# Optimization experiments

Measured on AMD Instinct MI355X. Metric: run time of the kernel, lower is better.

## Reference

```python
import jax, jax.numpy as jnp
import numpy as np

HIDDEN = 512
HORIZON = 24


def _cell(x, h, c, Wih, Whh, b):
    # PyTorch LSTM cell: gates ordered i, f, g, o; bias = b_ih + b_hh
    z = x @ Wih.T + h @ Whh.T + b  # [B, 4H]
    i, f, g, o = jnp.split(z, 4, axis=-1)
    c = jax.nn.sigmoid(f) * c + jax.nn.sigmoid(i) * jnp.tanh(g)
    h = jax.nn.sigmoid(o) * jnp.tanh(c)
    return h, c


def _run_layer(xs, Wih, Whh, b):
    # xs: [T, B, F] time-major; zero initial state like nn.LSTM
    B = xs.shape[1]
    H = Whh.shape[1]
    h0 = jnp.zeros((B, H), xs.dtype)
    c0 = jnp.zeros((B, H), xs.dtype)

    def step(carry, x_t):
        h, c = carry
        h, c = _cell(x_t, h, c, Wih, Whh, b)
        return (h, c), h

    (hT, cT), hs = jax.lax.scan(step, (h0, c0), xs)
    return hs, hT, cT


def setup_inputs() -> dict:
    key = jax.random.key(0)
    ks = jax.random.split(key, 20)
    s = 1.0 / np.sqrt(HIDDEN)  # torch LSTM/Linear default init scale
    u = lambda k, shape: jax.random.uniform(k, shape, jnp.float32, -s, s)
    B, T, F, H = 512, 256, 8, HIDDEN
    return {
        "x": jax.random.normal(ks[0], (B, T, F), jnp.float32),
        "e_Wih0": u(ks[1], (4 * H, F)),
        "e_Whh0": u(ks[2], (4 * H, H)),
        "e_bih0": u(ks[3], (4 * H,)),
        "e_bhh0": u(ks[4], (4 * H,)),
        "e_Wih1": u(ks[5], (4 * H, H)),
        "e_Whh1": u(ks[6], (4 * H, H)),
        "e_bih1": u(ks[7], (4 * H,)),
        "e_bhh1": u(ks[8], (4 * H,)),
        "d_Wih0": u(ks[9], (4 * H, 1)),
        "d_Whh0": u(ks[10], (4 * H, H)),
        "d_bih0": u(ks[11], (4 * H,)),
        "d_bhh0": u(ks[12], (4 * H,)),
        "d_Wih1": u(ks[13], (4 * H, H)),
        "d_Whh1": u(ks[14], (4 * H, H)),
        "d_bih1": u(ks[15], (4 * H,)),
        "d_bhh1": u(ks[16], (4 * H,)),
        "out_W": u(ks[17], (1, H)),
        "out_b": u(ks[18], (1,)),
    }


def reference(x, e_Wih0, e_Whh0, e_bih0, e_bhh0, e_Wih1, e_Whh1, e_bih1, e_bhh1,
              d_Wih0, d_Whh0, d_bih0, d_bhh0, d_Wih1, d_Whh1, d_bih1, d_bhh1,
              out_W, out_b):
    xs = jnp.swapaxes(x, 0, 1)  # [T, B, F]
    # 2-layer encoder; only final (hidden, cell) per layer are used
    hs0, h0T, c0T = _run_layer(xs, e_Wih0, e_Whh0, e_bih0 + e_bhh0)
    _, h1T, c1T = _run_layer(hs0, e_Wih1, e_Whh1, e_bih1 + e_bhh1)

    dec_in = x[:, -1, 0:1]  # [B, 1] last value of first feature channel

    def dec_step(carry, _):
        h0, c0, h1, c1, inp = carry
        h0, c0 = _cell(inp, h0, c0, d_Wih0, d_Whh0, d_bih0 + d_bhh0)
        h1, c1 = _cell(h0, h1, c1, d_Wih1, d_Whh1, d_bih1 + d_bhh1)
        pred = h1 @ out_W.T + out_b  # [B, 1]
        return (h0, c0, h1, c1, pred), pred

    carry = (h0T, c0T, h1T, c1T, dec_in)
    _, preds = jax.lax.scan(dec_step, carry, None, length=HORIZON)  # [Hz, B, 1]
    return jnp.swapaxes(preds[..., 0], 0, 1)  # [B, Hz]
```

## Files before the change

kernel.cpp:

```cpp
#include <hip/hip_runtime.h>
#include <math.h>

constexpr int H   = 512;
constexpr int B   = 512;
constexpr int T   = 256;
constexpr int F   = 8;
constexpr int HOR = 24;

typedef _Float16 f16;
typedef _Float16 f16x8 __attribute__((ext_vector_type(8)));
typedef float    f32x4 __attribute__((ext_vector_type(4)));

__device__ __forceinline__ float sigm(float x) { return 1.0f / (1.0f + expf(-x)); }

#define LLC_LOAD16S(base, r) \
  asm volatile( \
    "global_load_dwordx4 %0,  %16, off sc0 sc1\n\t" \
    "global_load_dwordx4 %1,  %16, off offset:16 sc0 sc1\n\t" \
    "global_load_dwordx4 %2,  %16, off offset:128 sc0 sc1\n\t" \
    "global_load_dwordx4 %3,  %16, off offset:144 sc0 sc1\n\t" \
    "global_load_dwordx4 %4,  %16, off offset:256 sc0 sc1\n\t" \
    "global_load_dwordx4 %5,  %16, off offset:272 sc0 sc1\n\t" \
    "global_load_dwordx4 %6,  %16, off offset:384 sc0 sc1\n\t" \
    "global_load_dwordx4 %7,  %16, off offset:400 sc0 sc1\n\t" \
    "global_load_dwordx4 %8,  %16, off offset:512 sc0 sc1\n\t" \
    "global_load_dwordx4 %9,  %16, off offset:528 sc0 sc1\n\t" \
    "global_load_dwordx4 %10, %16, off offset:640 sc0 sc1\n\t" \
    "global_load_dwordx4 %11, %16, off offset:656 sc0 sc1\n\t" \
    "global_load_dwordx4 %12, %16, off offset:768 sc0 sc1\n\t" \
    "global_load_dwordx4 %13, %16, off offset:784 sc0 sc1\n\t" \
    "global_load_dwordx4 %14, %16, off offset:896 sc0 sc1\n\t" \
    "global_load_dwordx4 %15, %16, off offset:912 sc0 sc1" \
    : "=v"(r[0]), "=v"(r[1]), "=v"(r[2]), "=v"(r[3]), \
      "=v"(r[4]), "=v"(r[5]), "=v"(r[6]), "=v"(r[7]), \
      "=v"(r[8]), "=v"(r[9]), "=v"(r[10]), "=v"(r[11]), \
      "=v"(r[12]), "=v"(r[13]), "=v"(r[14]), "=v"(r[15]) \
    : "v"(base))

#define VWAIT16(r) \
  asm volatile("s_waitcnt vmcnt(0)" \
    : "+v"(r[0]), "+v"(r[1]), "+v"(r[2]), "+v"(r[3]), \
      "+v"(r[4]), "+v"(r[5]), "+v"(r[6]), "+v"(r[7]), \
      "+v"(r[8]), "+v"(r[9]), "+v"(r[10]), "+v"(r[11]), \
      "+v"(r[12]), "+v"(r[13]), "+v"(r[14]), "+v"(r[15]) :: "memory")

#define LLC_STORE_DWX4(p, v) \
  asm volatile("global_store_dwordx4 %0, %1, off sc0 sc1" :: "v"(p), "v"(v) : "memory")

#define FLAG_STORE(p, v) \
  asm volatile("s_waitcnt vmcnt(0)\n\t" \
               "global_store_dword %0, %1, off sc0 sc1" :: "v"(p), "v"(v) : "memory")

__global__ __launch_bounds__(256)
void wconv_k(const float* __restrict__ s0, f16* __restrict__ d0,
             const float* __restrict__ s1, f16* __restrict__ d1,
             const float* __restrict__ s2, f16* __restrict__ d2,
             const float* __restrict__ s3, f16* __restrict__ d3,
             const float* __restrict__ s4, f16* __restrict__ d4,
             const float* __restrict__ s5, f16* __restrict__ d5)
{
    const float* src; f16* dst;
    switch (blockIdx.y) {
        case 0:  src = s0; dst = d0; break;
        case 1:  src = s1; dst = d1; break;
        case 2:  src = s2; dst = d2; break;
        case 3:  src = s3; dst = d3; break;
        case 4:  src = s4; dst = d4; break;
        default: src = s5; dst = d5; break;
    }
    int idx = (blockIdx.x * 256 + threadIdx.x) * 8;
    int np  = idx >> 9;
    int k   = idx & 511;
    int jh  = np >> 2, g = np & 3;
    const float* sp = src + (size_t)(g * H + jh) * H + k;
    f16 tmp[8];
    #pragma unroll
    for (int j = 0; j < 8; ++j) tmp[j] = (f16)sp[j];
    *(f16x8*)(dst + idx) = *(const f16x8*)tmp;
}

__device__ __forceinline__ void wait_group(const int* f, int target)
{
    if (threadIdx.x < 64) {
        const int* p = f + (threadIdx.x & 31);
        bool ok;
        do {
            int v = target;
            if (threadIdx.x < 32)
                asm volatile("global_load_dword %0, %1, off sc0 sc1\n\t"
                             "s_waitcnt vmcnt(0)"
                             : "=v"(v) : "v"(p) : "memory");
            ok = __all(v >= target);
            if (!ok) __builtin_amdgcn_s_sleep(1);
        } while (!ok);
    }
    __syncthreads();
}

struct WChunk { f16x8 w0, w1; };

__device__ __forceinline__ WChunk loadW(int kt, const f16* __restrict__ W0,
                                        const f16* __restrict__ W1,
                                        int n0, int srow, int sch)
{
    const f16* Wp = (kt < 8) ? W0 : W1;
    const int  ko = ((kt < 8) ? kt : kt - 8) * 64;
    const f16* wp = Wp + (size_t)(n0 + srow) * H + ko + sch * 16;
    WChunk c;
    c.w0 = *(const f16x8*)wp;
    c.w1 = *(const f16x8*)(wp + 8);
    return c;
}

template<int NKT>
__device__ __forceinline__ void cell_body(int bt, int nt, char* smem,
    const f16* __restrict__ A0, const f16* __restrict__ A1,
    const f16* __restrict__ W0, const f16* __restrict__ W1,
    const float* __restrict__ bih, const float* __restrict__ bhh,
    int xmode, const float* __restrict__ xptr, int xstride,
    const float* __restrict__ xw, const float* __restrict__ pred_s,
    float* __restrict__ cst, f16* __restrict__ hout)
{
    constexpr int ABUF = 64 * 72;
    f16*   As = (f16*)smem;
    f16*   Ws = (f16*)smem + 2 * ABUF;
    float* zs = (float*)smem;
    f16*   hstage = (f16*)(smem + 20480);

    const int tid  = threadIdx.x;
    const int lane = tid & 63;
    const int wv   = tid >> 6;
    const int wm   = wv & 1;
    const int wn   = wv >> 1;
    const int r    = lane & 15;
    const int g4   = lane >> 4;
    const int b0   = bt * 64;
    const int n0   = nt * 64;
    const int jh0  = nt * 16;
    const int srow = tid >> 2, sch = tid & 3;

    f32x4 acc[2][2] = {};

    if constexpr (NKT > 0) {
        f16x8 ar[16];
        f16x8 br[16];
        const f16* ap = A0 + (size_t)(b0 + srow) * H + sch * 16;
        LLC_LOAD16S(ap, ar);
        if constexpr (NKT == 16) {
            const f16* bp = A1 + (size_t)(b0 + srow) * H + sch * 16;
            LLC_LOAD16S(bp, br);
        }
        VWAIT16(ar);

        WChunk wcur = loadW(0, W0, W1, n0, srow, sch);
        #pragma unroll
        for (int kt = 0; kt < NKT; ++kt) {
            if (kt == 8) VWAIT16(br);
            f16* Ab = As + (kt & 1) * ABUF;
            f16* Wb = Ws + (kt & 1) * ABUF;
            f16x8 a0v = (kt < 8) ? ar[kt * 2]     : br[(kt - 8) * 2];
            f16x8 a1v = (kt < 8) ? ar[kt * 2 + 1] : br[(kt - 8) * 2 + 1];
            *(f16x8*)(Ab + srow * 72 + sch * 16)     = a0v;
            *(f16x8*)(Ab + srow * 72 + sch * 16 + 8) = a1v;
            *(f16x8*)(Wb + srow * 72 + sch * 16)     = wcur.w0;
            *(f16x8*)(Wb + srow * 72 + sch * 16 + 8) = wcur.w1;
            __syncthreads();

            WChunk wnxt = wcur;
            if (kt + 1 < NKT) wnxt = loadW(kt + 1, W0, W1, n0, srow, sch);

            #pragma unroll
            for (int sub = 0; sub < 2; ++sub) {
                f16x8 bf0 = *(const f16x8*)(Wb + (wn * 32 + r)      * 72 + sub * 32 + g4 * 8);
                f16x8 bf1 = *(const f16x8*)(Wb + (wn * 32 + 16 + r) * 72 + sub * 32 + g4 * 8);
                f16x8 af0 = *(const f16x8*)(Ab + (wm * 32 + r)      * 72 + sub * 32 + g4 * 8);
                f16x8 af1 = *(const f16x8*)(Ab + (wm * 32 + 16 + r) * 72 + sub * 32 + g4 * 8);
                acc[0][0] = __builtin_amdgcn_mfma_f32_16x16x32_f16(af0, bf0, acc[0][0], 0, 0, 0);
                acc[0][1] = __builtin_amdgcn_mfma_f32_16x16x32_f16(af0, bf1, acc[0][1], 0, 0, 0);
                acc[1][0] = __builtin_amdgcn_mfma_f32_16x16x32_f16(af1, bf0, acc[1][0], 0, 0, 0);
                acc[1][1] = __builtin_amdgcn_mfma_f32_16x16x32_f16(af1, bf1, acc[1][1], 0, 0, 0);
            }
            wcur = wnxt;
        }
    }

    __syncthreads();
    #pragma unroll
    for (int fm = 0; fm < 2; ++fm)
        #pragma unroll
        for (int fn = 0; fn < 2; ++fn)
            #pragma unroll
            for (int j = 0; j < 4; ++j)
                zs[(wm * 32 + fm * 16 + g4 * 4 + j) * 68 +
                   (wn * 32 + fn * 16 + r)] = acc[fm][fn][j];
    __syncthreads();

    const int jl = tid & 15;
    const int bq = tid >> 4;
    const int jh = jh0 + jl;

    float bsum[4];
    #pragma unroll
    for (int g = 0; g < 4; ++g) bsum[g] = bih[g * H + jh] + bhh[g * H + jh];

    #pragma unroll
    for (int bb = 0; bb < 4; ++bb) {
        const int bl = bq * 4 + bb;
        const int b  = b0 + bl;
        float4 z = *(const float4*)(zs + bl * 68 + jl * 4);
        float zi = z.x + bsum[0];
        float zf = z.y + bsum[1];
        float zg = z.z + bsum[2];
        float zo = z.w + bsum[3];
        if (xmode == 1) {
            const float* xr = xptr + (size_t)b * xstride;
            #pragma unroll
            for (int k = 0; k < F; ++k) {
                float xv = xr[k];
                zi += xv * xw[(0 * H + jh) * F + k];
                zf += xv * xw[(1 * H + jh) * F + k];
                zg += xv * xw[(2 * H + jh) * F + k];
                zo += xv * xw[(3 * H + jh) * F + k];
            }
        } else if (xmode == 2 || xmode == 3) {
            float xv = (xmode == 2) ? xptr[(size_t)b * xstride] : pred_s[bl];
            zi += xv * xw[0 * H + jh];
            zf += xv * xw[1 * H + jh];
            zg += xv * xw[2 * H + jh];
            zo += xv * xw[3 * H + jh];
        }
        size_t idx = (size_t)b * H + jh;
        float cold = cst[idx];
        float cn = sigm(zf) * cold + sigm(zi) * tanhf(zg);
        cst[idx] = cn;
        hstage[bl * 16 + jl] = (f16)(sigm(zo) * tanhf(cn));
    }
    __syncthreads();
    if (tid < 128) {
        const int row = tid >> 1, half = tid & 1;
        f16x8 hv = *(const f16x8*)(hstage + row * 16 + half * 8);
        f16* hp = hout + (size_t)(b0 + row) * H + jh0 + half * 8;
        LLC_STORE_DWX4(hp, hv);
    }
}

__device__ __forceinline__ void compute_pred(int bt, int nt,
                             const f16* __restrict__ h1src,
                             const float* __restrict__ outW,
                             const float* __restrict__ outb,
                             float* pred_s, float* __restrict__ dout, int oidx)
{
    const int row = threadIdx.x >> 2;
    const int q   = threadIdx.x & 3;
    const int b   = bt * 64 + row;
    const f16x8* hv = (const f16x8*)(h1src + (size_t)b * H + q * 128);
    float s = 0.f;
    #pragma unroll
    for (int k8 = 0; k8 < 16; ++k8) {
        f16x8 h8 = hv[k8];
        const float* wr = outW + q * 128 + k8 * 8;
        #pragma unroll
        for (int j = 0; j < 8; ++j) s += (float)h8[j] * wr[j];
    }
    s += __shfl_down(s, 2);
    s += __shfl_down(s, 1);
    if (q == 0) {
        float p = s + outb[0];
        pred_s[row] = p;
        if (nt == 0) dout[(size_t)b * HOR + oidx] = p;
    }
    __syncthreads();
}

struct PArgs {
    const f16 *wh0, *wih1, *whh1, *dwh0, *dwih1, *dwhh1;
    const float *x;
    const float *ebih0, *ebhh0, *ebih1, *ebhh1;
    const float *dbih0, *dbhh0, *dbih1, *dbhh1;
    const float *eWih0, *dWih0, *outW, *outb;
    f16 *h0ring, *h1ping, *h0dping, *h1dping;
    float *c0, *c1, *dout;
    int *f0, *f1;
};

__global__ __launch_bounds__(256, 2)
void enc2_k(PArgs a, int s)
{
    __shared__ __align__(16) char smem[37120];
    const size_t BH = (size_t)B * H;
    const int bid  = blockIdx.x;
    const int role = (bid >> 3) & 1;
    const int bt   = (bid >> 4) & 7;
    const int nt   = (bid & 7) | ((bid >> 7) << 3);
    int* const myf0 = a.f0 + bt * 32;
    int* const myf1 = a.f1 + bt * 32;
    const int t0 = 2 * s, t1 = 2 * s + 1;

    if (role == 0) {
        const f16* hp = a.h0ring + (size_t)((t0 + 3) & 3) * BH;
        f16* ho = a.h0ring + (size_t)(t0 & 3) * BH;
        if (t0 == 0)
            cell_body<0>(bt, nt, smem, hp, hp, a.wh0, a.wh0, a.ebih0, a.ebhh0,
                         1, a.x + (size_t)t0 * F, T * F, a.eWih0, nullptr, a.c0, ho);
        else
            cell_body<8>(bt, nt, smem, hp, hp, a.wh0, a.wh0, a.ebih0, a.ebhh0,
                         1, a.x + (size_t)t0 * F, T * F, a.eWih0, nullptr, a.c0, ho);
        __syncthreads();
        if (threadIdx.x == 0) FLAG_STORE(myf0 + nt, t0 + 1);
        wait_group(myf0, t0 + 1);
        cell_body<8>(bt, nt, smem, ho, ho, a.wh0, a.wh0, a.ebih0, a.ebhh0,
                     1, a.x + (size_t)t1 * F, T * F, a.eWih0, nullptr, a.c0,
                     a.h0ring + (size_t)(t1 & 3) * BH);
    } else {
        if (s > 0) {
            const int ta = 2 * s - 1;
            cell_body<16>(bt, nt, smem,
                          a.h0ring + (size_t)(ta & 3) * BH,
                          a.h1ping + (size_t)((ta + 1) & 1) * BH,
                          a.wih1, a.whh1, a.ebih1, a.ebhh1,
                          0, nullptr, 0, nullptr, nullptr,
                          a.c1, a.h1ping + (size_t)(ta & 1) * BH);
            __syncthreads();
            if (threadIdx.x == 0) FLAG_STORE(myf1 + nt, ta + 1);
        }
        const int tb = 2 * s;
        wait_group(myf0, tb + 1);
        if (s > 0) wait_group(myf1, tb);
        const f16* a0 = a.h0ring + (size_t)(tb & 3) * BH;
        f16* ho = a.h1ping + (size_t)(tb & 1) * BH;
        if (tb == 0)
            cell_body<8>(bt, nt, smem, a0, a0, a.wih1, a.wih1, a.ebih1, a.ebhh1,
                         0, nullptr, 0, nullptr, nullptr, a.c1, ho);
        else
            cell_body<16>(bt, nt, smem, a0,
                          a.h1ping + (size_t)((tb + 1) & 1) * BH,
                          a.wih1, a.whh1, a.ebih1, a.ebhh1,
                          0, nullptr, 0, nullptr, nullptr, a.c1, ho);
    }
}

__global__ __launch_bounds__(256, 2)
void enctail_k(PArgs a)
{
    __shared__ __align__(16) char smem[37120];
    const size_t BH = (size_t)B * H;
    const int bid = blockIdx.x;
    const int bt  = (bid >> 3) & 7;
    const int nt  = (bid & 7) | ((bid >> 6) << 3);
    cell_body<16>(bt, nt, smem,
                  a.h0ring + (size_t)3 * BH,
                  a.h1ping,
                  a.wih1, a.whh1, a.ebih1, a.ebhh1,
                  0, nullptr, 0, nullptr, nullptr,
                  a.c1, a.h1ping + BH);
}

__global__ __launch_bounds__(256, 2)
void dec0_k(PArgs a, int td)
{
    __shared__ __align__(16) char smem[37120];
    float* pred_s = (float*)(smem + 36864);
    const size_t BH = (size_t)B * H;
    const int bid = blockIdx.x;
    const int bt  = (bid >> 3) & 7;
    const int nt  = (bid & 7) | ((bid >> 6) << 3);

    if (td == 0) {
        const f16* hp = a.h0ring + (size_t)3 * BH;
        cell_body<8>(bt, nt, smem, hp, hp, a.dwh0, a.dwh0, a.dbih0, a.dbhh0,
                     2, a.x + (size_t)(T - 1) * F, T * F, a.dWih0, nullptr,
                     a.c0, a.h0dping);
    } else {
        compute_pred(bt, nt, a.h1dping + (size_t)((td + 1) & 1) * BH,
                     a.outW, a.outb, pred_s, a.dout, td - 1);
        const f16* hp = a.h0dping + (size_t)((td + 1) & 1) * BH;
        cell_body<8>(bt, nt, smem, hp, hp, a.dwh0, a.dwh0, a.dbih0, a.dbhh0,
                     3, nullptr, 0, a.dWih0, pred_s,
                     a.c0, a.h0dping + (size_t)(td & 1) * BH);
    }
}

__global__ __launch_bounds__(256, 2)
void dec1_k(PArgs a, int td)
{
    __shared__ __align__(16) char smem[37120];
    const size_t BH = (size_t)B * H;
    const int bid = blockIdx.x;
    const int bt  = (bid >> 3) & 7;
    const int nt  = (bid & 7) | ((bid >> 6) << 3);
    const f16* a1 = (td == 0) ? a.h1ping + BH
                              : a.h1dping + (size_t)((td + 1) & 1) * BH;
    cell_body<16>(bt, nt, smem, a.h0dping + (size_t)(td & 1) * BH, a1,
                  a.dwih1, a.dwhh1, a.dbih1, a.dbhh1,
                  0, nullptr, 0, nullptr, nullptr,
                  a.c1, a.h1dping + (size_t)(td & 1) * BH);
}

__global__ __launch_bounds__(256)
void predf_k(const f16* __restrict__ h1, const float* __restrict__ outW,
             const float* __restrict__ outb, float* __restrict__ dout)
{
    int wv = threadIdx.x >> 6, lane = threadIdx.x & 63;
    int b = blockIdx.x * 4 + wv;
    const f16* hr = h1 + (size_t)b * H;
    float s = 0.f;
    #pragma unroll
    for (int k = 0; k < H; k += 64) s += (float)hr[k + lane] * outW[k + lane];
    #pragma unroll
    for (int off = 32; off > 0; off >>= 1) s += __shfl_down(s, off);
    if (lane == 0) dout[(size_t)b * HOR + (HOR - 1)] = s + outb[0];
}

extern "C" void kernel_launch(void* const* d_in, const int* in_sizes, int n_in,
                              void* d_out, int out_size, void* d_ws, size_t ws_size,
                              hipStream_t stream)
{
    const float* x     = (const float*)d_in[0];
    const float* eWih0 = (const float*)d_in[1];
    const float* eWhh0 = (const float*)d_in[2];
    const float* ebih0 = (const float*)d_in[3];
    const float* ebhh0 = (const float*)d_in[4];
    const float* eWih1 = (const float*)d_in[5];
    const float* eWhh1 = (const float*)d_in[6];
    const float* ebih1 = (const float*)d_in[7];
    const float* ebhh1 = (const float*)d_in[8];
    const float* dWih0 = (const float*)d_in[9];
    const float* dWhh0 = (const float*)d_in[10];
    const float* dbih0 = (const float*)d_in[11];
    const float* dbhh0 = (const float*)d_in[12];
    const float* dWih1 = (const float*)d_in[13];
    const float* dWhh1 = (const float*)d_in[14];
    const float* dbih1 = (const float*)d_in[15];
    const float* dbhh1 = (const float*)d_in[16];
    const float* outW  = (const float*)d_in[17];
    const float* outb  = (const float*)d_in[18];

    const size_t WSZ = (size_t)4 * H * H;
    const size_t BH  = (size_t)B * H;

    char* wsb = (char*)d_ws;
    size_t off = 0;
    f16* wh[6];
    for (int i = 0; i < 6; ++i) { wh[i] = (f16*)(wsb + off); off += WSZ * sizeof(f16); }
    f16* h0ring  = (f16*)(wsb + off); off += 4 * BH * sizeof(f16);
    f16* h1ping  = (f16*)(wsb + off); off += 2 * BH * sizeof(f16);
    f16* h0dping = (f16*)(wsb + off); off += 2 * BH * sizeof(f16);
    f16* h1dping = (f16*)(wsb + off); off += 2 * BH * sizeof(f16);
    float* c0    = (float*)(wsb + off); off += BH * sizeof(float);
    float* c1    = (float*)(wsb + off); off += BH * sizeof(float);
    size_t coff  = off;
    int* f0      = (int*)(wsb + off); off += 8 * 32 * sizeof(int);
    int* f1      = (int*)(wsb + off); off += 8 * 32 * sizeof(int);
    size_t cbytes = off - coff;

    wconv_k<<<dim3(512, 6), 256, 0, stream>>>(eWhh0, wh[0], eWih1, wh[1], eWhh1, wh[2],
                                              dWhh0, wh[3], dWih1, wh[4], dWhh1, wh[5]);
    hipMemsetAsync(c0, 0, BH * sizeof(float), stream);
    hipMemsetAsync(c1, 0, BH * sizeof(float), stream);
    hipMemsetAsync((char*)wsb + coff, 0, cbytes, stream);

    PArgs a;
    a.wh0 = wh[0]; a.wih1 = wh[1]; a.whh1 = wh[2];
    a.dwh0 = wh[3]; a.dwih1 = wh[4]; a.dwhh1 = wh[5];
    a.x = x;
    a.ebih0 = ebih0; a.ebhh0 = ebhh0; a.ebih1 = ebih1; a.ebhh1 = ebhh1;
    a.dbih0 = dbih0; a.dbhh0 = dbhh0; a.dbih1 = dbih1; a.dbhh1 = dbhh1;
    a.eWih0 = eWih0; a.dWih0 = dWih0; a.outW = outW; a.outb = outb;
    a.h0ring = h0ring; a.h1ping = h1ping; a.h0dping = h0dping; a.h1dping = h1dping;
    a.c0 = c0; a.c1 = c1; a.dout = (float*)d_out;
    a.f0 = f0; a.f1 = f1;

    for (int s = 0; s < T / 2; ++s)
        enc2_k<<<dim3(512), dim3(256), 0, stream>>>(a, s);
    enctail_k<<<dim3(256), dim3(256), 0, stream>>>(a);

    for (int td = 0; td < HOR; ++td) {
        dec0_k<<<dim3(256), dim3(256), 0, stream>>>(a, td);
        dec1_k<<<dim3(256), dim3(256), 0, stream>>>(a, td);
    }
    predf_k<<<dim3(128), dim3(256), 0, stream>>>(h1dping + BH, outW, outb, (float*)d_out);
}
```

Before: 4.519 ms.

## Fuse decoder layer kernels with flag sync, transpose x, merge encoder waits

Merges the two per-step decoder kernels into one 512-block launch in which layer-0 blocks publish per-batch-tile flags and layer-1 blocks spin-wait on them, halving decoder launch count. Adds a pre-transpose of x to time-feature-major layout so encoder layer-0 x loads are coalesced across batch. Combines the two encoder flag waits into a single polling loop. The fused decoder relies on all 512 blocks being co-resident; otherwise spinning blocks could delay or deadlock.

Result: slower. 4.808 ms (+6.4%).

```diff
diff --git a/kernel.cpp b/kernel.cpp
--- a/kernel.cpp
+++ b/kernel.cpp
@@ -79,6 +79,16 @@
     *(f16x8*)(dst + idx) = *(const f16x8*)tmp;
 }
 
+__global__ __launch_bounds__(256)
+void xpose_k(const float* __restrict__ x, float* __restrict__ xT)
+{
+    int idx = blockIdx.x * 256 + threadIdx.x;
+    int b  = idx & (B - 1);
+    int tk = idx >> 9;
+    int t  = tk >> 3, k = tk & 7;
+    xT[idx] = x[(size_t)b * T * F + t * F + k];
+}
+
 __device__ __forceinline__ void wait_group(const int* f, int target)
 {
     if (threadIdx.x < 64) {
@@ -91,6 +101,26 @@
                              "s_waitcnt vmcnt(0)"
                              : "=v"(v) : "v"(p) : "memory");
             ok = __all(v >= target);
+            if (!ok) __builtin_amdgcn_s_sleep(1);
+        } while (!ok);
+    }
+    __syncthreads();
+}
+
+__device__ __forceinline__ void wait_two(const int* fA, int tA,
+                                         const int* fB, int tB)
+{
+    if (threadIdx.x < 64) {
+        const int l = threadIdx.x;
+        const int* p = (l < 32) ? fA + l : fB + (l - 32);
+        const int tgt = (l < 32) ? tA : tB;
+        bool ok;
+        do {
+            int v;
+            asm volatile("global_load_dword %0, %1, off sc0 sc1\n\t"
+                         "s_waitcnt vmcnt(0)"
+                         : "=v"(v) : "v"(p) : "memory");
+            ok = __all(v >= tgt);
             if (!ok) __builtin_amdgcn_s_sleep(1);
         } while (!ok);
     }
@@ -213,10 +243,9 @@
         float zg = z.z + bsum[2];
         float zo = z.w + bsum[3];
         if (xmode == 1) {
-            const float* xr = xptr + (size_t)b * xstride;
             #pragma unroll
             for (int k = 0; k < F; ++k) {
-                float xv = xr[k];
+                float xv = xptr[(size_t)k * B + b];
                 zi += xv * xw[(0 * H + jh) * F + k];
                 zf += xv * xw[(1 * H + jh) * F + k];
                 zg += xv * xw[(2 * H + jh) * F + k];
@@ -274,13 +303,13 @@
 
 struct PArgs {
     const f16 *wh0, *wih1, *whh1, *dwh0, *dwih1, *dwhh1;
-    const float *x;
+    const float *x, *xT;
     const float *ebih0, *ebhh0, *ebih1, *ebhh1;
     const float *dbih0, *dbhh0, *dbih1, *dbhh1;
     const float *eWih0, *dWih0, *outW, *outb;
     f16 *h0ring, *h1ping, *h0dping, *h1dping;
     float *c0, *c1, *dout;
-    int *f0, *f1;
+    int *f0, *f1, *f0d;
 };
 
 __global__ __launch_bounds__(256, 2)
@@ -301,15 +330,15 @@
         f16* ho = a.h0ring + (size_t)(t0 & 3) * BH;
         if (t0 == 0)
             cell_body<0>(bt, nt, smem, hp, hp, a.wh0, a.wh0, a.ebih0, a.ebhh0,
-                         1, a.x + (size_t)t0 * F, T * F, a.eWih0, nullptr, a.c0, ho);
+                         1, a.xT + (size_t)t0 * F * B, 0, a.eWih0, nullptr, a.c0, ho);
         else
             cell_body<8>(bt, nt, smem, hp, hp, a.wh0, a.wh0, a.ebih0, a.ebhh0,
-                         1, a.x + (size_t)t0 * F, T * F, a.eWih0, nullptr, a.c0, ho);
+                         1, a.xT + (size_t)t0 * F * B, 0, a.eWih0, nullptr, a.c0, ho);
         __syncthreads();
         if (threadIdx.x == 0) FLAG_STORE(myf0 + nt, t0 + 1);
         wait_group(myf0, t0 + 1);
         cell_body<8>(bt, nt, smem, ho, ho, a.wh0, a.wh0, a.ebih0, a.ebhh0,
-                     1, a.x + (size_t)t1 * F, T * F, a.eWih0, nullptr, a.c0,
+                     1, a.xT + (size_t)t1 * F * B, 0, a.eWih0, nullptr, a.c0,
                      a.h0ring + (size_t)(t1 & 3) * BH);
     } else {
         if (s > 0) {
@@ -324,8 +353,8 @@
             if (threadIdx.x == 0) FLAG_STORE(myf1 + nt, ta + 1);
         }
         const int tb = 2 * s;
-        wait_group(myf0, tb + 1);
-        if (s > 0) wait_group(myf1, tb);
+        if (s > 0) wait_two(myf0, tb + 1, myf1, tb);
+        else       wait_group(myf0, tb + 1);
         const f16* a0 = a.h0ring + (size_t)(tb & 3) * BH;
         f16* ho = a.h1ping + (size_t)(tb & 1) * BH;
         if (tb == 0)
@@ -356,44 +385,42 @@
 }
 
 __global__ __launch_bounds__(256, 2)
-void dec0_k(PArgs a, int td)
+void dec_k(PArgs a, int td)
 {
     __shared__ __align__(16) char smem[37120];
     float* pred_s = (float*)(smem + 36864);
     const size_t BH = (size_t)B * H;
-    const int bid = blockIdx.x;
-    const int bt  = (bid >> 3) & 7;
-    const int nt  = (bid & 7) | ((bid >> 6) << 3);
-
-    if (td == 0) {
-        const f16* hp = a.h0ring + (size_t)3 * BH;
-        cell_body<8>(bt, nt, smem, hp, hp, a.dwh0, a.dwh0, a.dbih0, a.dbhh0,
-                     2, a.x + (size_t)(T - 1) * F, T * F, a.dWih0, nullptr,
-                     a.c0, a.h0dping);
+    const int bid  = blockIdx.x;
+    const int role = (bid >> 3) & 1;
+    const int bt   = (bid >> 4) & 7;
+    const int nt   = (bid & 7) | ((bid >> 7) << 3);
+    int* const myf0d = a.f0d + bt * 32;
+
+    if (role == 0) {
+        if (td == 0) {
+            const f16* hp = a.h0ring + (size_t)3 * BH;
+            cell_body<8>(bt, nt, smem, hp, hp, a.dwh0, a.dwh0, a.dbih0, a.dbhh0,
+                         2, a.x + (size_t)(T - 1) * F, T * F, a.dWih0, nullptr,
+                         a.c0, a.h0dping);
+        } else {
+            compute_pred(bt, nt, a.h1dping + (size_t)((td + 1) & 1) * BH,
+                         a.outW, a.outb, pred_s, a.dout, td - 1);
+            const f16* hp = a.h0dping + (size_t)((td + 1) & 1) * BH;
+            cell_body<8>(bt, nt, smem, hp, hp, a.dwh0, a.dwh0, a.dbih0, a.dbhh0,
+                         3, nullptr, 0, a.dWih0, pred_s,
+                         a.c0, a.h0dping + (size_t)(td & 1) * BH);
+        }
+        __syncthreads();
+        if (threadIdx.x == 0) FLAG_STORE(myf0d + nt, td + 1);
     } else {
-        compute_pred(bt, nt, a.h1dping + (size_t)((td + 1) & 1) * BH,
-                     a.outW, a.outb, pred_s, a.dout, td - 1);
-        const f16* hp = a.h0dping + (size_t)((td + 1) & 1) * BH;
-        cell_body<8>(bt, nt, smem, hp, hp, a.dwh0, a.dwh0, a.dbih0, a.dbhh0,
-                     3, nullptr, 0, a.dWih0, pred_s,
-                     a.c0, a.h0dping + (size_t)(td & 1) * BH);
-    }
-}
-
-__global__ __launch_bounds__(256, 2)
-void dec1_k(PArgs a, int td)
-{
-    __shared__ __align__(16) char smem[37120];
-    const size_t BH = (size_t)B * H;
-    const int bid = blockIdx.x;
-    const int bt  = (bid >> 3) & 7;
-    const int nt  = (bid & 7) | ((bid >> 6) << 3);
-    const f16* a1 = (td == 0) ? a.h1ping + BH
-                              : a.h1dping + (size_t)((td + 1) & 1) * BH;
-    cell_body<16>(bt, nt, smem, a.h0dping + (size_t)(td & 1) * BH, a1,
-                  a.dwih1, a.dwhh1, a.dbih1, a.dbhh1,
-                  0, nullptr, 0, nullptr, nullptr,
-                  a.c1, a.h1dping + (size_t)(td & 1) * BH);
+        wait_group(myf0d, td + 1);
+        const f16* a1 = (td == 0) ? a.h1ping + BH
+                                  : a.h1dping + (size_t)((td + 1) & 1) * BH;
+        cell_body<16>(bt, nt, smem, a.h0dping + (size_t)(td & 1) * BH, a1,
+                      a.dwih1, a.dwhh1, a.dbih1, a.dbhh1,
+                      0, nullptr, 0, nullptr, nullptr,
+                      a.c1, a.h1dping + (size_t)(td & 1) * BH);
+    }
 }
 
 __global__ __launch_bounds__(256)
@@ -448,13 +475,16 @@
     f16* h1dping = (f16*)(wsb + off); off += 2 * BH * sizeof(f16);
     float* c0    = (float*)(wsb + off); off += BH * sizeof(float);
     float* c1    = (float*)(wsb + off); off += BH * sizeof(float);
+    float* xT    = (float*)(wsb + off); off += (size_t)T * F * B * sizeof(float);
     size_t coff  = off;
     int* f0      = (int*)(wsb + off); off += 8 * 32 * sizeof(int);
     int* f1      = (int*)(wsb + off); off += 8 * 32 * sizeof(int);
+    int* f0d     = (int*)(wsb + off); off += 8 * 32 * sizeof(int);
     size_t cbytes = off - coff;
 
     wconv_k<<<dim3(512, 6), 256, 0, stream>>>(eWhh0, wh[0], eWih1, wh[1], eWhh1, wh[2],
                                               dWhh0, wh[3], dWih1, wh[4], dWhh1, wh[5]);
+    xpose_k<<<dim3((T * F * B) / 256), 256, 0, stream>>>(x, xT);
     hipMemsetAsync(c0, 0, BH * sizeof(float), stream);
     hipMemsetAsync(c1, 0, BH * sizeof(float), stream);
     hipMemsetAsync((char*)wsb + coff, 0, cbytes, stream);
@@ -462,21 +492,19 @@
     PArgs a;
     a.wh0 = wh[0]; a.wih1 = wh[1]; a.whh1 = wh[2];
     a.dwh0 = wh[3]; a.dwih1 = wh[4]; a.dwhh1 = wh[5];
-    a.x = x;
+    a.x = x; a.xT = xT;
     a.ebih0 = ebih0; a.ebhh0 = ebhh0; a.ebih1 = ebih1; a.ebhh1 = ebhh1;
     a.dbih0 = dbih0; a.dbhh0 = dbhh0; a.dbih1 = dbih1; a.dbhh1 = dbhh1;
     a.eWih0 = eWih0; a.dWih0 = dWih0; a.outW = outW; a.outb = outb;
     a.h0ring = h0ring; a.h1ping = h1ping; a.h0dping = h0dping; a.h1dping = h1dping;
     a.c0 = c0; a.c1 = c1; a.dout = (float*)d_out;
-    a.f0 = f0; a.f1 = f1;
+    a.f0 = f0; a.f1 = f1; a.f0d = f0d;
 
     for (int s = 0; s < T / 2; ++s)
         enc2_k<<<dim3(512), dim3(256), 0, stream>>>(a, s);
     enctail_k<<<dim3(256), dim3(256), 0, stream>>>(a);
 
-    for (int td = 0; td < HOR; ++td) {
-        dec0_k<<<dim3(256), dim3(256), 0, stream>>>(a, td);
-        dec1_k<<<dim3(256), dim3(256), 0, stream>>>(a, td);
-    }
+    for (int td = 0; td < HOR; ++td)
+        dec_k<<<dim3(512), dim3(256), 0, stream>>>(a, td);
     predf_k<<<dim3(128), dim3(256), 0, stream>>>(h1dping + BH, outW, outb, (float*)d_out);
 }
```
